# Kernel optimization log

Measured on AMD Instinct MI355X. Metric: run time of the kernel, lower is better.

## Reference

```python
import jax, jax.numpy as jnp
import numpy as np

B, D = 4096, 768

def setup_inputs() -> dict:
    key = jax.random.key(0)
    k1, k2 = jax.random.split(key)
    embeddings = jax.random.normal(k1, (B, D), dtype=jnp.float32)
    # precomputed articulatory distance matrix (stand-in for articulatory_distance_fn over word pairs)
    art_dist = jax.random.uniform(k2, (B, B), dtype=jnp.float32)
    return {"embeddings": embeddings, "art_dist": art_dist}

def reference(embeddings, art_dist):
    b = embeddings.shape[0]
    # pairwise squared L2 distances via Gram matrix: ||ei||^2 + ||ej||^2 - 2 ei.ej
    sq = jnp.sum(embeddings * embeddings, axis=1)                  # [B]
    gram = jnp.einsum('id,jd->ij', embeddings, embeddings)         # [B, B]
    d2 = sq[:, None] + sq[None, :] - 2.0 * gram                    # [B, B]
    off_diag = 1.0 - jnp.eye(b, dtype=embeddings.dtype)            # exclude i == j
    pair_loss = (d2 - art_dist) ** 2
    pairs_count = b * (b - 1)
    return jnp.sum(pair_loss * off_diag) / pairs_count
```

## Files before the change

### kernel.cpp

```cpp
#include <hip/hip_runtime.h>
#include <hip/hip_bf16.h>

#define B_DIM 4096
#define D_DIM 768
#define BM 128
#define BN 128
#define BK 64
#define NT (B_DIM / BM)

typedef __bf16 bf16_t;
typedef bf16_t bf16x8 __attribute__((ext_vector_type(8)));
typedef float f32x4 __attribute__((ext_vector_type(4)));

static __device__ __forceinline__ ushort f2bf(float v) {
    __hip_bfloat16 h = __float2bfloat16(v);
    return *reinterpret_cast<const ushort*>(&h);
}

__global__ __launch_bounds__(256) void prep_kernel(
    const float* __restrict__ E, ushort* __restrict__ Ebf, float* __restrict__ sq)
{
    const int lane = threadIdx.x & 63;
    const int row  = blockIdx.x * 4 + (threadIdx.x >> 6);
    const float4* er = reinterpret_cast<const float4*>(E + (size_t)row * D_DIM);
    ushort4* br = reinterpret_cast<ushort4*>(Ebf + (size_t)row * D_DIM);
    float s = 0.f;
    #pragma unroll
    for (int k = 0; k < 3; ++k) {
        float4 v = er[lane + 64 * k];
        s += v.x * v.x + v.y * v.y + v.z * v.z + v.w * v.w;
        ushort4 o;
        o.x = f2bf(v.x); o.y = f2bf(v.y); o.z = f2bf(v.z); o.w = f2bf(v.w);
        br[lane + 64 * k] = o;
    }
    #pragma unroll
    for (int off = 32; off > 0; off >>= 1) s += __shfl_down(s, off);
    if (lane == 0) sq[row] = s;
}

__global__ __launch_bounds__(256, 4) void gram_loss_kernel(
    const ushort* __restrict__ Ebf, const float* __restrict__ sq,
    const float* __restrict__ art, float* __restrict__ out)
{
    __shared__ ushort Als[BM][BK];
    __shared__ ushort Bls[BN][BK];
    __shared__ float red[4];

    const int tid  = threadIdx.x;
    const int lane = tid & 63;
    const int wave = tid >> 6;
    const int wr = wave >> 1;
    const int wc = wave & 1;

    const int swz = (blockIdx.x & 7) * 128 + (blockIdx.x >> 3);
    const int tileR = swz >> 5;
    const int tileC = swz & 31;
    const int row0 = tileR * BM;
    const int col0 = tileC * BN;

    f32x4 acc[4][4] = {};

    const int srow  = tid >> 3;
    const int scol8 = (tid & 7) * 8;

    for (int kk = 0; kk < D_DIM; kk += BK) {
        #pragma unroll
        for (int i = 0; i < 4; ++i) {
            const int r = i * 32 + srow;
            const int colg = scol8 ^ ((r & 7) << 3);
            const ushort* gA = Ebf + (size_t)(row0 + r) * D_DIM + kk + colg;
            __builtin_amdgcn_global_load_lds(
                (const __attribute__((address_space(1))) void*)gA,
                (__attribute__((address_space(3))) void*)(&Als[r][scol8]),
                16, 0, 0);
            const ushort* gB = Ebf + (size_t)(col0 + r) * D_DIM + kk + colg;
            __builtin_amdgcn_global_load_lds(
                (const __attribute__((address_space(1))) void*)gB,
                (__attribute__((address_space(3))) void*)(&Bls[r][scol8]),
                16, 0, 0);
        }
        __syncthreads();

        #pragma unroll
        for (int k2 = 0; k2 < BK; k2 += 32) {
            bf16x8 af[4], bfr[4];
            #pragma unroll
            for (int m = 0; m < 4; ++m) {
                const int r = wr * 64 + m * 16 + (lane & 15);
                const int c = (k2 + (lane >> 4) * 8) ^ ((r & 7) << 3);
                af[m] = *reinterpret_cast<const bf16x8*>(&Als[r][c]);
            }
            #pragma unroll
            for (int n = 0; n < 4; ++n) {
                const int r = wc * 64 + n * 16 + (lane & 15);
                const int c = (k2 + (lane >> 4) * 8) ^ ((r & 7) << 3);
                bfr[n] = *reinterpret_cast<const bf16x8*>(&Bls[r][c]);
            }
            #pragma unroll
            for (int m = 0; m < 4; ++m)
                #pragma unroll
                for (int n = 0; n < 4; ++n)
                    acc[m][n] = __builtin_amdgcn_mfma_f32_16x16x32_bf16(
                        af[m], bfr[n], acc[m][n], 0, 0, 0);
        }
        __syncthreads();
    }

    float lsum = 0.f;
    const int lr = (lane >> 4) * 4;
    const int lc = lane & 15;
    const int rbase = row0 + wr * 64;
    const int cbase = col0 + wc * 64;

    if (tileR != tileC) {
        #pragma unroll
        for (int m = 0; m < 4; ++m) {
            const int gi0 = rbase + m * 16 + lr;
            float sqi[4];
            #pragma unroll
            for (int j = 0; j < 4; ++j) sqi[j] = sq[gi0 + j];
            #pragma unroll
            for (int n = 0; n < 4; ++n) {
                const int gj = cbase + n * 16 + lc;
                const float sqj = sq[gj];
                const float4 am = *reinterpret_cast<const float4*>(
                    &art[(size_t)gj * B_DIM + gi0]);
                const float amv[4] = { am.x, am.y, am.z, am.w };
                #pragma unroll
                for (int j = 0; j < 4; ++j) {
                    const float d2 = sqi[j] + sqj - 2.0f * acc[m][n][j];
                    const float t = d2 - amv[j];
                    lsum += t * t;
                }
            }
        }
    } else {
        #pragma unroll
        for (int m = 0; m < 4; ++m) {
            const int gi0 = rbase + m * 16 + lr;
            float sqi[4];
            #pragma unroll
            for (int j = 0; j < 4; ++j) sqi[j] = sq[gi0 + j];
            #pragma unroll
            for (int n = 0; n < 4; ++n) {
                const int gj = cbase + n * 16 + lc;
                const float sqj = sq[gj];
                const float4 am = *reinterpret_cast<const float4*>(
                    &art[(size_t)gj * B_DIM + gi0]);
                const float amv[4] = { am.x, am.y, am.z, am.w };
                #pragma unroll
                for (int j = 0; j < 4; ++j) {
                    const int gi = gi0 + j;
                    const float d2 = sqi[j] + sqj - 2.0f * acc[m][n][j];
                    const float t = d2 - amv[j];
                    if (gi != gj) lsum += t * t;
                }
            }
        }
    }

    #pragma unroll
    for (int off = 32; off > 0; off >>= 1) lsum += __shfl_down(lsum, off);
    if (lane == 0) red[wave] = lsum;
    __syncthreads();
    if (tid == 0) {
        const float inv_pairs = 1.0f / ((float)B_DIM * (float)(B_DIM - 1));
        atomicAdd(out, (red[0] + red[1] + red[2] + red[3]) * inv_pairs);
    }
}

extern "C" void kernel_launch(void* const* d_in, const int* in_sizes, int n_in,
                              void* d_out, int out_size, void* d_ws, size_t ws_size,
                              hipStream_t stream) {
    const float* E   = (const float*)d_in[0];
    const float* art = (const float*)d_in[1];
    float* out = (float*)d_out;

    ushort* Ebf = (ushort*)d_ws;
    float*  sq  = (float*)((char*)d_ws + (size_t)B_DIM * D_DIM * 2);

    hipMemsetAsync(d_out, 0, sizeof(float), stream);
    prep_kernel<<<B_DIM / 4, 256, 0, stream>>>(E, Ebf, sq);
    gram_loss_kernel<<<NT * NT, 256, 0, stream>>>(Ebf, sq, art, out);
}
```

Before: 129.4 us.

## Use 256x256 tiles with double-buffered async LDS prefetch interleaved with MFMA

Replaces the 128x128 Gram tile with a 256x256 tile computed by 512 threads, using 128 KB of dynamic LDS as two buffers. The next K-chunk is loaded straight into LDS and those loads are interleaved with four MFMA phases, paced by manual vmcnt waits and barriers, with raised wave priority around the MFMA bursts. The aim is to hide global load latency behind compute and to halve redundant reads of the bf16 embeddings. The trade-offs are a grid of only 256 blocks, roughly one per CU, so the strided art-reading epilogue no longer overlaps with other blocks' GEMM work, plus higher register pressure from the 8x4 accumulators.

```diff
diff --git a/kernel.cpp b/kernel.cpp
--- a/kernel.cpp
+++ b/kernel.cpp
@@ -3,10 +3,10 @@
 
 #define B_DIM 4096
 #define D_DIM 768
-#define BM 128
-#define BN 128
+#define BM 256
 #define BK 64
-#define NT (B_DIM / BM)
+#define NSTEP (D_DIM / BK)
+#define NTI (B_DIM / BM)
 
 typedef __bf16 bf16_t;
 typedef bf16_t bf16x8 __attribute__((ext_vector_type(8)));
@@ -38,87 +38,133 @@
     if (lane == 0) sq[row] = s;
 }
 
-__global__ __launch_bounds__(256, 4) void gram_loss_kernel(
+template<int P>
+__device__ __forceinline__ void issue_chunk(
+    const ushort* __restrict__ Ebf, ushort* lbase, int panel_row0, int kkn, int tid)
+{
+    #pragma unroll
+    for (int q = 0; q < 2; ++q) {
+        const int idx = q * 512 + tid;
+        const int rl  = idx >> 3;
+        const int c16 = idx & 7;
+        int r;
+        if      (P == 1) r = rl + (rl & 64);
+        else if (P == 2) r = 64 + rl + (rl & 64);
+        else if (P == 3) r = ((rl >> 5) << 6) + (rl & 31);
+        else             r = ((rl >> 5) << 6) + 32 + (rl & 31);
+        const int cg = (c16 ^ (r & 7)) << 3;
+        const ushort* gsrc = Ebf + (size_t)(panel_row0 + r) * D_DIM + kkn + cg;
+        ushort* ldst = lbase + r * 64 + c16 * 8;
+        __builtin_amdgcn_global_load_lds(
+            (const __attribute__((address_space(1))) void*)gsrc,
+            (__attribute__((address_space(3))) void*)ldst, 16, 0, 0);
+    }
+}
+
+template<int QM, int QN>
+__device__ __forceinline__ void phase_mfma(
+    const ushort* Acur, const ushort* Bcur, f32x4 (&acc)[8][4],
+    int wr, int wc, int lane)
+{
+    bf16x8 af[4][2], bv[2][2];
+    const int l15 = lane & 15;
+    const int kq  = (lane >> 4) * 8;
+    #pragma unroll
+    for (int mm = 0; mm < 4; ++mm)
+        #pragma unroll
+        for (int k2 = 0; k2 < 2; ++k2) {
+            const int ra = wr * 128 + QM * 64 + mm * 16 + l15;
+            const int c  = (k2 * 32 + kq) ^ ((ra & 7) << 3);
+            af[mm][k2] = *reinterpret_cast<const bf16x8*>(Acur + ra * 64 + c);
+        }
+    #pragma unroll
+    for (int nn = 0; nn < 2; ++nn)
+        #pragma unroll
+        for (int k2 = 0; k2 < 2; ++k2) {
+            const int rb = wc * 64 + QN * 32 + nn * 16 + l15;
+            const int c  = (k2 * 32 + kq) ^ ((rb & 7) << 3);
+            bv[nn][k2] = *reinterpret_cast<const bf16x8*>(Bcur + rb * 64 + c);
+        }
+    __builtin_amdgcn_s_setprio(1);
+    #pragma unroll
+    for (int mm = 0; mm < 4; ++mm)
+        #pragma unroll
+        for (int nn = 0; nn < 2; ++nn)
+            #pragma unroll
+            for (int k2 = 0; k2 < 2; ++k2)
+                acc[QM * 4 + mm][QN * 2 + nn] = __builtin_amdgcn_mfma_f32_16x16x32_bf16(
+                    af[mm][k2], bv[nn][k2], acc[QM * 4 + mm][QN * 2 + nn], 0, 0, 0);
+    __builtin_amdgcn_s_setprio(0);
+}
+
+__global__ __launch_bounds__(512, 2) void gram_loss_kernel(
     const ushort* __restrict__ Ebf, const float* __restrict__ sq,
     const float* __restrict__ art, float* __restrict__ out)
 {
-    __shared__ ushort Als[BM][BK];
-    __shared__ ushort Bls[BN][BK];
-    __shared__ float red[4];
+    extern __shared__ char smem[];
+    ushort* Ab = (ushort*)smem;
+    ushort* Bb = (ushort*)(smem + 65536);
+    float*  red = (float*)(smem + 131072);
 
     const int tid  = threadIdx.x;
     const int lane = tid & 63;
     const int wave = tid >> 6;
-    const int wr = wave >> 1;
-    const int wc = wave & 1;
-
-    const int swz = (blockIdx.x & 7) * 128 + (blockIdx.x >> 3);
-    const int tileR = swz >> 5;
-    const int tileC = swz & 31;
+    const int wr = wave >> 2;
+    const int wc = wave & 3;
+
+    const int swz = (blockIdx.x & 7) * 32 + (blockIdx.x >> 3);
+    const int tileR = swz >> 4;
+    const int tileC = swz & 15;
     const int row0 = tileR * BM;
-    const int col0 = tileC * BN;
-
-    f32x4 acc[4][4] = {};
-
-    const int srow  = tid >> 3;
-    const int scol8 = (tid & 7) * 8;
-
-    for (int kk = 0; kk < D_DIM; kk += BK) {
-        #pragma unroll
-        for (int i = 0; i < 4; ++i) {
-            const int r = i * 32 + srow;
-            const int colg = scol8 ^ ((r & 7) << 3);
-            const ushort* gA = Ebf + (size_t)(row0 + r) * D_DIM + kk + colg;
-            __builtin_amdgcn_global_load_lds(
-                (const __attribute__((address_space(1))) void*)gA,
-                (__attribute__((address_space(3))) void*)(&Als[r][scol8]),
-                16, 0, 0);
-            const ushort* gB = Ebf + (size_t)(col0 + r) * D_DIM + kk + colg;
-            __builtin_amdgcn_global_load_lds(
-                (const __attribute__((address_space(1))) void*)gB,
-                (__attribute__((address_space(3))) void*)(&Bls[r][scol8]),
-                16, 0, 0);
-        }
-        __syncthreads();
-
-        #pragma unroll
-        for (int k2 = 0; k2 < BK; k2 += 32) {
-            bf16x8 af[4], bfr[4];
-            #pragma unroll
-            for (int m = 0; m < 4; ++m) {
-                const int r = wr * 64 + m * 16 + (lane & 15);
-                const int c = (k2 + (lane >> 4) * 8) ^ ((r & 7) << 3);
-                af[m] = *reinterpret_cast<const bf16x8*>(&Als[r][c]);
-            }
-            #pragma unroll
-            for (int n = 0; n < 4; ++n) {
-                const int r = wc * 64 + n * 16 + (lane & 15);
-                const int c = (k2 + (lane >> 4) * 8) ^ ((r & 7) << 3);
-                bfr[n] = *reinterpret_cast<const bf16x8*>(&Bls[r][c]);
-            }
-            #pragma unroll
-            for (int m = 0; m < 4; ++m)
-                #pragma unroll
-                for (int n = 0; n < 4; ++n)
-                    acc[m][n] = __builtin_amdgcn_mfma_f32_16x16x32_bf16(
-                        af[m], bfr[n], acc[m][n], 0, 0, 0);
-        }
-        __syncthreads();
+    const int col0 = tileC * BM;
+
+    f32x4 acc[8][4] = {};
+
+    issue_chunk<1>(Ebf, Ab, row0, 0, tid);
+    issue_chunk<2>(Ebf, Ab, row0, 0, tid);
+    issue_chunk<3>(Ebf, Bb, col0, 0, tid);
+    issue_chunk<4>(Ebf, Bb, col0, 0, tid);
+
+    #pragma unroll 2
+    for (int s = 0; s < NSTEP; ++s) {
+        const int b = s & 1;
+        const int kkn = ((s + 1) % NSTEP) * BK;
+        const ushort* Acur = Ab + b * 16384;
+        const ushort* Bcur = Bb + b * 16384;
+        ushort* Anxt = Ab + (b ^ 1) * 16384;
+        ushort* Bnxt = Bb + (b ^ 1) * 16384;
+
+        asm volatile("s_waitcnt vmcnt(2)" ::: "memory");
+        __builtin_amdgcn_s_barrier();
+        __builtin_amdgcn_sched_barrier(0);
+
+        issue_chunk<1>(Ebf, Anxt, row0, kkn, tid);
+        phase_mfma<0, 0>(Acur, Bcur, acc, wr, wc, lane);
+        issue_chunk<2>(Ebf, Anxt, row0, kkn, tid);
+        phase_mfma<1, 0>(Acur, Bcur, acc, wr, wc, lane);
+
+        asm volatile("s_waitcnt vmcnt(4)" ::: "memory");
+        __builtin_amdgcn_s_barrier();
+        __builtin_amdgcn_sched_barrier(0);
+
+        issue_chunk<3>(Ebf, Bnxt, col0, kkn, tid);
+        phase_mfma<0, 1>(Acur, Bcur, acc, wr, wc, lane);
+        issue_chunk<4>(Ebf, Bnxt, col0, kkn, tid);
+        phase_mfma<1, 1>(Acur, Bcur, acc, wr, wc, lane);
     }
 
     float lsum = 0.f;
     const int lr = (lane >> 4) * 4;
     const int lc = lane & 15;
-    const int rbase = row0 + wr * 64;
+    const int rbase = row0 + wr * 128;
     const int cbase = col0 + wc * 64;
 
     if (tileR != tileC) {
         #pragma unroll
-        for (int m = 0; m < 4; ++m) {
+        for (int m = 0; m < 8; ++m) {
             const int gi0 = rbase + m * 16 + lr;
-            float sqi[4];
-            #pragma unroll
-            for (int j = 0; j < 4; ++j) sqi[j] = sq[gi0 + j];
+            const float4 sqv = *reinterpret_cast<const float4*>(sq + gi0);
+            const float sqi[4] = { sqv.x, sqv.y, sqv.z, sqv.w };
             #pragma unroll
             for (int n = 0; n < 4; ++n) {
                 const int gj = cbase + n * 16 + lc;
@@ -136,11 +182,10 @@
         }
     } else {
         #pragma unroll
-        for (int m = 0; m < 4; ++m) {
+        for (int m = 0; m < 8; ++m) {
             const int gi0 = rbase + m * 16 + lr;
-            float sqi[4];
-            #pragma unroll
-            for (int j = 0; j < 4; ++j) sqi[j] = sq[gi0 + j];
+            const float4 sqv = *reinterpret_cast<const float4*>(sq + gi0);
+            const float sqi[4] = { sqv.x, sqv.y, sqv.z, sqv.w };
             #pragma unroll
             for (int n = 0; n < 4; ++n) {
                 const int gj = cbase + n * 16 + lc;
@@ -164,8 +209,11 @@
     if (lane == 0) red[wave] = lsum;
     __syncthreads();
     if (tid == 0) {
+        float tot = 0.f;
+        #pragma unroll
+        for (int w = 0; w < 8; ++w) tot += red[w];
         const float inv_pairs = 1.0f / ((float)B_DIM * (float)(B_DIM - 1));
-        atomicAdd(out, (red[0] + red[1] + red[2] + red[3]) * inv_pairs);
+        atomicAdd(out, tot * inv_pairs);
     }
 }
 
@@ -179,7 +227,11 @@
     ushort* Ebf = (ushort*)d_ws;
     float*  sq  = (float*)((char*)d_ws + (size_t)B_DIM * D_DIM * 2);
 
+    const int lds_bytes = 131072 + 256;
+    (void)hipFuncSetAttribute((const void*)gram_loss_kernel,
+                              hipFuncAttributeMaxDynamicSharedMemorySize, lds_bytes);
+
     hipMemsetAsync(d_out, 0, sizeof(float), stream);
     prep_kernel<<<B_DIM / 4, 256, 0, stream>>>(E, Ebf, sq);
-    gram_loss_kernel<<<NT * NT, 256, 0, stream>>>(Ebf, sq, art, out);
-}
+    gram_loss_kernel<<<NTI * NTI, 512, lds_bytes, stream>>>(Ebf, sq, art, out);
+}
```

New measurement: 129.4 us. About the same (-0.0%).
